# Optimization experiments

Hardware: AMD Instinct MI355X
Metric: run time of the kernel (lower is better)

Reference implementation:

```python
import jax, jax.numpy as jnp
import numpy as np

B, C, N, L = 64, 32, 500, 12
C_OUT = 32
C_CAT = 9 * C  # (order*(support_len+1)+1)*c_in = 288


def setup_inputs() -> dict:
    key = jax.random.key(0)
    ks = jax.random.split(key, 7)
    x = jax.random.normal(ks[0], (B, C, N, L), dtype=jnp.float32)
    # row-stochastic-ish adjacencies: scale by 1/N to keep hops numerically tame
    A0 = jax.random.uniform(ks[1], (N, N), dtype=jnp.float32) / N
    A1 = jax.random.uniform(ks[2], (N, N), dtype=jnp.float32) / N
    A2 = jax.random.uniform(ks[3], (N, N), dtype=jnp.float32) / N
    A3 = jax.random.uniform(ks[4], (B, N, N), dtype=jnp.float32) / N
    W = jax.random.normal(ks[5], (C_OUT, C_CAT), dtype=jnp.float32) * 0.05
    b = jax.random.normal(ks[6], (C_OUT,), dtype=jnp.float32) * 0.05
    return {"x": x, "A0": A0, "A1": A1, "A2": A2, "A3": A3, "W": W, "b": b}


def reference(x, A0, A1, A2, A3, W, b):
    # x: [B, C, N, L]; A0..A2: [N, N]; A3: [B, N, N]; W: [C_OUT, 9*C]; b: [C_OUT]
    def hop2(h, A):  # static adjacency
        return jnp.einsum('ncvl,vw->ncwl', h, A)

    def hop3(h, A):  # batched (dynamic) adjacency
        return jnp.einsum('ncvl,nvw->ncwl', h, A)

    out = [x]
    for A in (A0, A1, A2):
        x1 = hop2(x, A)
        x2 = hop2(x1, A)
        out.extend([x1, x2])
    x1 = hop3(x, A3)
    x2 = hop3(x1, A3)
    out.extend([x1, x2])

    h = jnp.concatenate(out, axis=1)  # [B, 9C, N, L]
    # 1x1 Conv2d == channel mixing matmul + bias
    h = jnp.einsum('ncvl,oc->novl', h, W) + b[None, :, None, None]
    # dropout in eval mode: identity
    return h
```

## Files before the change

kernel.cpp:

```cpp
#include <hip/hip_runtime.h>

typedef unsigned short u16;
typedef __bf16 bf16x8 __attribute__((ext_vector_type(8)));
typedef float f32x4 __attribute__((ext_vector_type(4)));
typedef const unsigned int __attribute__((address_space(1))) gu32;
typedef unsigned int __attribute__((address_space(3))) lu32;

#define NN 500
#define LLc 12
#define CC 32
#define MM 384
#define KP 512
#define MT 96
#define NT2 128
#define XS_S 40
#define AS_S 40
#define CT2_S 136
#define TS_S 384
#define AT_ELS 256000

__device__ __forceinline__ u16 f2bf(float f) {
    union { float f; unsigned u; } cv; cv.f = f;
    unsigned u = cv.u;
    u += 0x7fffu + ((u >> 16) & 1u);
    return (u16)(u >> 16);
}
__device__ __forceinline__ float bf2f(u16 s) {
    union { unsigned u; float f; } cv; cv.u = ((unsigned)s) << 16;
    return cv.f;
}

__global__ __launch_bounds__(256) void atrans_all(
    const float* __restrict__ A0, const float* __restrict__ A1,
    const float* __restrict__ A2, const float* __restrict__ A3,
    u16* __restrict__ At_s, u16* __restrict__ At_b)
{
    __shared__ u16 Ls[32 * 36];
    const int t = threadIdx.x;
    const int n0 = blockIdx.x * 32;
    const int k0 = blockIdx.y * 32;
    const int z = blockIdx.z;
    const float* Ab; u16* Ob;
    if (z == 0)      { Ab = A0; Ob = At_s; }
    else if (z == 1) { Ab = A1; Ob = At_s + (long)AT_ELS; }
    else if (z == 2) { Ab = A2; Ob = At_s + 2L * AT_ELS; }
    else             { Ab = A3 + (long)(z - 3) * NN * NN; Ob = At_b + (long)(z - 3) * AT_ELS; }
    {
        int vl = t >> 3, u = t & 7;
        float4 v = make_float4(0.f, 0.f, 0.f, 0.f);
        if (k0 + vl < NN && n0 + 4 * u + 4 <= NN)
            v = *(const float4*)(Ab + (long)(k0 + vl) * NN + n0 + 4 * u);
        int nb = 4 * u;
        Ls[(nb + 0) * 36 + vl] = f2bf(v.x);
        Ls[(nb + 1) * 36 + vl] = f2bf(v.y);
        Ls[(nb + 2) * 36 + vl] = f2bf(v.z);
        Ls[(nb + 3) * 36 + vl] = f2bf(v.w);
    }
    __syncthreads();
    {
        int row = t >> 3, u = t & 7;
        if (n0 + row < NN)
            *(uint2*)(Ob + (long)(n0 + row) * KP + k0 + 4 * u) = *(const uint2*)(&Ls[row * 36 + 4 * u]);
    }
}

__global__ __launch_bounds__(256) void xpose_kernel(
    const float* __restrict__ x, u16* __restrict__ Xt)
{
    __shared__ u16 Ls[MM * 36];
    const int t = threadIdx.x;
    const int v0 = blockIdx.x * 32;
    const int b  = blockIdx.y;
    #pragma unroll
    for (int j = 0; j < 12; ++j) {
        int f = t + 256 * j;
        int c = f / 96;
        int r = f - c * 96;
        int vl = r / 3;
        int l3 = (r - vl * 3) * 4;
        float4 v = make_float4(0.f, 0.f, 0.f, 0.f);
        if (v0 + vl < NN)
            v = *(const float4*)(x + ((long)b * CC + c) * (NN * LLc) + (long)(v0 + vl) * LLc + l3);
        int mb = (c * LLc + l3) * 36 + vl;
        Ls[mb]       = f2bf(v.x);
        Ls[mb + 36]  = f2bf(v.y);
        Ls[mb + 72]  = f2bf(v.z);
        Ls[mb + 108] = f2bf(v.w);
    }
    __syncthreads();
    #pragma unroll
    for (int j = 0; j < 12; ++j) {
        int f = t + 256 * j;
        int row = f >> 3, u = f & 7;
        *(uint2*)(Xt + ((long)b * MM + row) * KP + v0 + 4 * u) = *(const uint2*)(&Ls[row * 36 + 4 * u]);
    }
}

__global__ __launch_bounds__(256) void wpack_kernel(
    const float* __restrict__ W, u16* __restrict__ Wp)
{
    const int t = threadIdx.x;
    #pragma unroll 1
    for (int k = 0; k < 72; ++k) {
        int idx = t + 256 * k;
        int j    = idx & 7;
        int lane = (idx >> 3) & 63;
        int p    = (idx >> 9) & 1;
        int mt   = (idx >> 10) & 1;
        int g    = idx >> 11;
        int o  = mt * 16 + (lane & 15);
        int kk = g * 32 + (lane >> 4) * 8 + j;
        float wv = W[o * 288 + kk];
        u16 hi = f2bf(wv);
        Wp[idx] = (p == 0) ? hi : f2bf(wv - bf2f(hi));
    }
}

__global__ __launch_bounds__(256, 4) void hop_fast2(
    const u16* __restrict__ Xsrc, long x_gstride, long x_bstride, int x_rstride, int x_klim,
    const u16* __restrict__ At_s,
    const u16* __restrict__ At_b,
    u16* __restrict__ Hout, long h_gstride)
{
    __shared__ __align__(16) u16 smem[13056];
    u16* As = smem;
    u16* Xs = smem + 5120;
    u16* Ct = smem;

    const int t = threadIdx.x;
    const int lane = t & 63;
    const int wv = t >> 6;
    const int n0 = blockIdx.x * NT2;
    const int m0 = blockIdx.y * MT;
    const int g  = blockIdx.z & 3;
    const int b  = blockIdx.z >> 2;
    const int ln = lane & 15;
    const int q8 = (lane >> 4) * 8;

    const u16* Ab = (g < 3) ? (At_s + (long)g * AT_ELS) : (At_b + (long)b * AT_ELS);
    const u16* Xb = Xsrc + (long)g * x_gstride + (long)b * x_bstride;
    u16* Ob = Hout + (long)g * h_gstride + (long)b * ((long)MM * NN);

    uint2 pa[4], px[3];
    auto loadA = [&](int k0) {
        #pragma unroll
        for (int j = 0; j < 4; ++j) {
            int f = t + 256 * j;
            int n = f >> 3, u = f & 7;
            uint2 v = make_uint2(0u, 0u);
            if (n0 + n < NN)
                v = *(const uint2*)(Ab + (long)(n0 + n) * KP + k0 + 4 * u);
            pa[j] = v;
        }
    };
    auto loadX = [&](int k0) {
        #pragma unroll
        for (int j = 0; j < 3; ++j) {
            int f = t + 256 * j;
            int r = f >> 3, u = f & 7;
            int k = k0 + 4 * u;
            uint2 v = make_uint2(0u, 0u);
            if (k < x_klim)
                v = *(const uint2*)(Xb + (long)(m0 + r) * x_rstride + k);
            px[j] = v;
        }
    };

    f32x4 acc[2][6];
    #pragma unroll
    for (int ns = 0; ns < 2; ++ns)
        #pragma unroll
        for (int i = 0; i < 6; ++i)
            #pragma unroll
            for (int r = 0; r < 4; ++r) acc[ns][i][r] = 0.f;

    loadA(0);
    loadX(0);
    #pragma unroll 1
    for (int s = 0; s < 16; ++s) {
        __syncthreads();
        #pragma unroll
        for (int j = 0; j < 4; ++j) {
            int f = t + 256 * j;
            *(uint2*)(&As[(f >> 3) * AS_S + 4 * (f & 7)]) = pa[j];
        }
        #pragma unroll
        for (int j = 0; j < 3; ++j) {
            int f = t + 256 * j;
            *(uint2*)(&Xs[(f >> 3) * XS_S + 4 * (f & 7)]) = px[j];
        }
        if (s < 15) {
            loadA(32 * (s + 1));
            loadX(32 * (s + 1));
        }
        __syncthreads();
        bf16x8 af[6];
        #pragma unroll
        for (int i = 0; i < 6; ++i)
            af[i] = *(const bf16x8*)(&Xs[(i * 16 + ln) * XS_S + q8]);
        #pragma unroll
        for (int ns = 0; ns < 2; ++ns) {
            bf16x8 bfr = *(const bf16x8*)(&As[(wv * 32 + ns * 16 + ln) * AS_S + q8]);
            #pragma unroll
            for (int i = 0; i < 6; ++i)
                acc[ns][i] = __builtin_amdgcn_mfma_f32_16x16x32_bf16(af[i], bfr, acc[ns][i], 0, 0, 0);
        }
    }

    __syncthreads();
    #pragma unroll
    for (int ns = 0; ns < 2; ++ns) {
        int col = wv * 32 + ns * 16 + ln;
        #pragma unroll
        for (int i = 0; i < 6; ++i) {
            int rb = i * 16 + (lane >> 4) * 4;
            #pragma unroll
            for (int r = 0; r < 4; ++r)
                Ct[(rb + r) * CT2_S + col] = f2bf(acc[ns][i][r]);
        }
    }
    __syncthreads();
    #pragma unroll
    for (int j = 0; j < 12; ++j) {
        int f = t + 256 * j;
        int row = f >> 5, u = f & 31;
        int n = n0 + 4 * u;
        if (n < NN)
            *(uint2*)(Ob + (long)(m0 + row) * NN + n) = *(const uint2*)(&Ct[row * CT2_S + 4 * u]);
    }
}

__global__ __launch_bounds__(512, 4) void mix_mfma(
    const u16* __restrict__ Xt,
    const u16* __restrict__ H,
    const u16* __restrict__ Wp,
    const float* __restrict__ bias,
    float* __restrict__ out)
{
    __shared__ __align__(16) char smem[50176];
    u16*   Ls = (u16*)smem;
    float* Ct = (float*)smem;

    const int t   = threadIdx.x;
    const int wg  = blockIdx.y * 8 + blockIdx.x;
    const int swz = (wg & 7) * 64 + (wg >> 3);
    const int bx  = swz & 7;
    const int b   = swz >> 3;
    const int n0  = bx * 64;
    const int w    = t >> 6;
    const int lane = t & 63;
    const int kq   = lane >> 4;
    const int ln   = lane & 15;
    const int srow   = lane >> 3;
    const int schunk = (lane & 7) * 8;

    f32x4 acc[6][2];
    #pragma unroll
    for (int i = 0; i < 6; ++i)
        #pragma unroll
        for (int m = 0; m < 2; ++m)
            #pragma unroll
            for (int r = 0; r < 4; ++r) acc[i][m][r] = 0.f;

    #pragma unroll 1
    for (int g = 0; g < 9; ++g) {
        const u16* base; int rs;
        if (g == 0) { base = Xt + (long)b * (MM * KP); rs = KP; }
        else {
            int gg = g - 1;
            int buf = (gg & 1) ? 4 + (gg >> 1) : (gg >> 1);
            base = H + (long)buf * 12288000L + (long)b * 192000L; rs = NN;
        }
        __syncthreads();
        #pragma unroll
        for (int i = 0; i < 6; ++i) {
            int r0 = (w * 6 + i) * 8;
            const u16* src = base + (long)(r0 + srow) * rs + n0 + schunk;
            __builtin_amdgcn_global_load_lds((gu32*)src, (lu32*)(Ls + r0 * 64), 16, 0, 0);
        }
        asm volatile("s_waitcnt vmcnt(0)" ::: "memory");
        __syncthreads();
        uint4 wf[2][2];
        #pragma unroll
        for (int mt = 0; mt < 2; ++mt)
            #pragma unroll
            for (int p = 0; p < 2; ++p)
                wf[mt][p] = *(const uint4*)(Wp + ((((g * 2 + mt) * 2 + p) * 64 + lane) * 8));
        #pragma unroll
        for (int i = 0; i < 6; ++i) {
            int ct = w * 6 + i;
            int off0 = kq * 6144 + (ct >> 2) * 64 + (ct & 3) * 16 + ln;
            union { u16 s[8]; bf16x8 v; } fb;
            #pragma unroll
            for (int j = 0; j < 8; ++j) fb.s[j] = Ls[off0 + j * 768];
            #pragma unroll
            for (int mt = 0; mt < 2; ++mt) {
                acc[i][mt] = __builtin_amdgcn_mfma_f32_16x16x32_bf16(*(const bf16x8*)&wf[mt][0], fb.v, acc[i][mt], 0, 0, 0);
                acc[i][mt] = __builtin_amdgcn_mfma_f32_16x16x32_bf16(*(const bf16x8*)&wf[mt][1], fb.v, acc[i][mt], 0, 0, 0);
            }
        }
    }

    #pragma unroll
    for (int mt = 0; mt < 2; ++mt) {
        __syncthreads();
        #pragma unroll
        for (int i = 0; i < 6; ++i) {
            int col = (w * 6 + i) * 16 + ln;
            #pragma unroll
            for (int r = 0; r < 4; ++r)
                Ct[(kq * 4 + r) * 781 + col] = acc[i][mt][r];
        }
        __syncthreads();
        int o16 = t >> 5, u = t & 31;
        int og = mt * 16 + o16;
        float bs = bias[og];
        float* ob = out + (((long)b * CC + og) * NN + n0) * 12L;
        #pragma unroll
        for (int j2 = 0; j2 < 2; ++j2) {
            int n = u + 32 * j2;
            if (n0 + n < NN) {
                float v[12];
                #pragma unroll
                for (int l = 0; l < 12; ++l) v[l] = Ct[o16 * 781 + l * 64 + n] + bs;
                #pragma unroll
                for (int q = 0; q < 3; ++q)
                    *(float4*)(ob + (long)n * 12 + q * 4) = *(const float4*)&v[q * 4];
            }
        }
    }
}

__global__ __launch_bounds__(256, 3) void mix_all(
    const u16* __restrict__ Xt,
    const u16* __restrict__ H,
    const float* __restrict__ W,
    const float* __restrict__ bias,
    float* __restrict__ out)
{
    __shared__ __align__(16) float smem[96 * 36 + 288 * 33];
    float* ts = smem;
    float* Ws = smem + 96 * 36;

    const int t  = threadIdx.x;
    const int b  = blockIdx.y;
    const int w0 = blockIdx.x * 32;
    const int o  = t & 31;
    const int wq = t >> 5;
    const int w4 = wq * 4;
    const long HBUF = (long)64 * MM * NN;

    #pragma unroll
    for (int j = 0; j < 36; ++j) {
        int f = t + 256 * j;
        int oo = f & 31, ci = f >> 5;
        Ws[ci * 33 + oo] = W[oo * 288 + ci];
    }

    float acc[4][12];
    #pragma unroll
    for (int k = 0; k < 4; ++k)
        #pragma unroll
        for (int l = 0; l < 12; ++l) acc[k][l] = 0.f;

    uint2 px[3];
    auto loadq = [&](int q) {
        int g = q >> 2, c0 = (q & 3) << 3;
        const u16* base; int rs;
        if (g == 0) { base = Xt + (long)b * (MM * KP); rs = KP; }
        else {
            int gg = g - 1, i = gg >> 1;
            int buf = (gg & 1) ? 4 + i : i;
            base = H + (long)buf * HBUF + (long)b * ((long)MM * NN); rs = NN;
        }
        int m0c = c0 * 12;
        #pragma unroll
        for (int j = 0; j < 3; ++j) {
            int f = t + 256 * j;
            int r = f >> 3, u = f & 7;
            px[j] = *(const uint2*)(base + (long)(m0c + r) * rs + w0 + 4 * u);
        }
    };

    loadq(0);
    #pragma unroll 1
    for (int q = 0; q < 36; ++q) {
        __syncthreads();
        #pragma unroll
        for (int j = 0; j < 3; ++j) {
            int f = t + 256 * j;
            int r = f >> 3, u = f & 7;
            uint2 raw = px[j];
            float4 v = make_float4(bf2f((u16)(raw.x & 0xffffu)), bf2f((u16)(raw.x >> 16)),
                                   bf2f((u16)(raw.y & 0xffffu)), bf2f((u16)(raw.y >> 16)));
            *(float4*)(&ts[r * 36 + 4 * u]) = v;
        }
        if (q < 35) loadq(q + 1);
        __syncthreads();
        int g = q >> 2, c0 = (q & 3) << 3;
        #pragma unroll 1
        for (int cl = 0; cl < 8; ++cl) {
            float wgt = Ws[(g * 32 + c0 + cl) * 33 + o];
            #pragma unroll
            for (int l = 0; l < 12; ++l) {
                float4 h = *(const float4*)(&ts[(cl * 12 + l) * 36 + w4]);
                acc[0][l] += wgt * h.x;
                acc[1][l] += wgt * h.y;
                acc[2][l] += wgt * h.z;
                acc[3][l] += wgt * h.w;
            }
        }
    }

    #pragma unroll 1
    for (int r = 0; r < 4; ++r) {
        __syncthreads();
        if ((o >> 3) == r) {
            int ol = o & 7;
            #pragma unroll
            for (int k = 0; k < 4; ++k)
                #pragma unroll
                for (int l = 0; l < 12; ++l)
                    ts[ol * 388 + (w4 + k) * 12 + l] = acc[k][l];
        }
        __syncthreads();
        #pragma unroll
        for (int j = 0; j < 3; ++j) {
            int f4 = t + 256 * j;
            int ol = f4 / 96;
            int rem = f4 - ol * 96;
            int w  = rem / 3;
            int lq = rem - w * 3;
            if (w0 + w < NN) {
                float4 v = *(const float4*)(&ts[ol * 388 + w * 12 + lq * 4]);
                float bs = bias[r * 8 + ol];
                v.x += bs; v.y += bs; v.z += bs; v.w += bs;
                *(float4*)(out + (((long)b * CC + r * 8 + ol) * NN + w0 + w) * LLc + lq * 4) = v;
            }
        }
    }
}

__global__ __launch_bounds__(256, 4) void hop_fast(
    const u16* __restrict__ Xsrc, long x_bstride, int x_rstride, int x_klim,
    const u16* __restrict__ At,   long a_bstride,
    u16* __restrict__ hout)
{
    __shared__ __align__(16) u16 smem[13056];
    u16* As = smem;
    u16* Xs = smem + 5120;
    u16* Ct = smem;

    const int t = threadIdx.x;
    const int lane = t & 63;
    const int wv = t >> 6;
    const int n0 = blockIdx.x * NT2;
    const int m0 = blockIdx.y * MT;
    const int b  = blockIdx.z;
    const int ln = lane & 15;
    const int q8 = (lane >> 4) * 8;

    const u16* Ab = At + (long)b * a_bstride;
    const u16* Xb = Xsrc + (long)b * x_bstride;

    uint2 pa[4], px[3];
    auto loadA = [&](int k0) {
        #pragma unroll
        for (int j = 0; j < 4; ++j) {
            int f = t + 256 * j;
            int n = f >> 3, u = f & 7;
            uint2 v = make_uint2(0u, 0u);
            if (n0 + n < NN)
                v = *(const uint2*)(Ab + (long)(n0 + n) * KP + k0 + 4 * u);
            pa[j] = v;
        }
    };
    auto loadX = [&](int k0) {
        #pragma unroll
        for (int j = 0; j < 3; ++j) {
            int f = t + 256 * j;
            int r = f >> 3, u = f & 7;
            int k = k0 + 4 * u;
            uint2 v = make_uint2(0u, 0u);
            if (k < x_klim)
                v = *(const uint2*)(Xb + (long)(m0 + r) * x_rstride + k);
            px[j] = v;
        }
    };

    f32x4 acc[2][6];
    #pragma unroll
    for (int ns = 0; ns < 2; ++ns)
        #pragma unroll
        for (int i = 0; i < 6; ++i)
            #pragma unroll
            for (int r = 0; r < 4; ++r) acc[ns][i][r] = 0.f;

    loadA(0);
    loadX(0);
    #pragma unroll 1
    for (int s = 0; s < 16; ++s) {
        __syncthreads();
        #pragma unroll
        for (int j = 0; j < 4; ++j) {
            int f = t + 256 * j;
            *(uint2*)(&As[(f >> 3) * AS_S + 4 * (f & 7)]) = pa[j];
        }
        #pragma unroll
        for (int j = 0; j < 3; ++j) {
            int f = t + 256 * j;
            *(uint2*)(&Xs[(f >> 3) * XS_S + 4 * (f & 7)]) = px[j];
        }
        if (s < 15) {
            loadA(32 * (s + 1));
            loadX(32 * (s + 1));
        }
        __syncthreads();
        bf16x8 af[6];
        #pragma unroll
        for (int i = 0; i < 6; ++i)
            af[i] = *(const bf16x8*)(&Xs[(i * 16 + ln) * XS_S + q8]);
        #pragma unroll
        for (int ns = 0; ns < 2; ++ns) {
            bf16x8 bfr = *(const bf16x8*)(&As[(wv * 32 + ns * 16 + ln) * AS_S + q8]);
            #pragma unroll
            for (int i = 0; i < 6; ++i)
                acc[ns][i] = __builtin_amdgcn_mfma_f32_16x16x32_bf16(af[i], bfr, acc[ns][i], 0, 0, 0);
        }
    }

    __syncthreads();
    #pragma unroll
    for (int ns = 0; ns < 2; ++ns) {
        int col = wv * 32 + ns * 16 + ln;
        #pragma unroll
        for (int i = 0; i < 6; ++i) {
            int rb = i * 16 + (lane >> 4) * 4;
            #pragma unroll
            for (int r = 0; r < 4; ++r)
                Ct[(rb + r) * CT2_S + col] = f2bf(acc[ns][i][r]);
        }
    }
    __syncthreads();
    u16* Ob = hout + (long)b * ((long)MM * NN);
    #pragma unroll
    for (int j = 0; j < 12; ++j) {
        int f = t + 256 * j;
        int row = f >> 5, u = f & 31;
        int n = n0 + 4 * u;
        if (n < NN)
            *(uint2*)(Ob + (long)(m0 + row) * NN + n) = *(const uint2*)(&Ct[row * CT2_S + 4 * u]);
    }
}

__global__ __launch_bounds__(256, 2) void mix_kernel(
    const float* __restrict__ x,
    const u16* __restrict__ h1,
    const u16* __restrict__ h2,
    const float* __restrict__ W,
    const float* __restrict__ bias,
    int blk1, int blk2,
    float* __restrict__ out, int init)
{
    __shared__ __align__(16) float smem[CC * TS_S + 3 * 1056];
    float* ts = smem;
    float* Ws = smem + CC * TS_S;

    const int t = threadIdx.x;
    const int b = blockIdx.y;
    const int w0 = blockIdx.x * 32;
    const int o  = t & 15;
    const int wg = (t >> 4) & 7;
    const int lh = t >> 7;

    #pragma unroll
    for (int j = 0; j < 4; ++j) {
        int f = t + 256 * j;
        int oo = f & 31, c = f >> 5;
        Ws[c * 33 + oo]        = W[oo * 288 + blk1 * 32 + c];
        Ws[1056 + c * 33 + oo] = W[oo * 288 + blk2 * 32 + c];
        if (init) Ws[2112 + c * 33 + oo] = W[oo * 288 + c];
    }

    float acc2[2][4][6];
    #pragma unroll
    for (int a = 0; a < 2; ++a)
        #pragma unroll
        for (int q = 0; q < 4; ++q)
            #pragma unroll
            for (int l = 0; l < 6; ++l) acc2[a][q][l] = 0.f;

    auto stage_h = [&](const u16* h) {
        #pragma unroll
        for (int j = 0; j < 12; ++j) {
            int f = t + 256 * j;
            int row = f >> 3, u = f & 7;
            int w = w0 + 4 * u;
            uint2 raw = make_uint2(0u, 0u);
            if (w < NN)
                raw = *(const uint2*)(h + ((long)b * MM + row) * NN + w);
            int c = row / 12;
            int l = row - c * 12;
            float* dst = &ts[c * TS_S + l * 32 + 4 * u];
            dst[0] = bf2f((u16)(raw.x & 0xffffu));
            dst[1] = bf2f((u16)(raw.x >> 16));
            dst[2] = bf2f((u16)(raw.y & 0xffffu));
            dst[3] = bf2f((u16)(raw.y >> 16));
        }
    };
    auto accum = [&](const float* Wg) {
        for (int c = 0; c < CC; ++c) {
            float w1 = Wg[c * 33 + o];
            float w2 = Wg[c * 33 + o + 16];
            #pragma unroll
            for (int l6 = 0; l6 < 6; ++l6) {
                const float4 hv = *(const float4*)(&ts[c * TS_S + (lh * 6 + l6) * 32 + wg * 4]);
                acc2[0][0][l6] += w1 * hv.x;
                acc2[0][1][l6] += w1 * hv.y;
                acc2[0][2][l6] += w1 * hv.z;
                acc2[0][3][l6] += w1 * hv.w;
                acc2[1][0][l6] += w2 * hv.x;
                acc2[1][1][l6] += w2 * hv.y;
                acc2[1][2][l6] += w2 * hv.z;
                acc2[1][3][l6] += w2 * hv.w;
            }
        }
    };

    if (init) {
        #pragma unroll
        for (int j = 0; j < 12; ++j) {
            int f = t + 256 * j;
            int c = f / 96;
            int r = f - c * 96;
            int w = r / 3;
            int q = r - w * 3;
            float4 v = make_float4(0.f, 0.f, 0.f, 0.f);
            if (w0 + w < NN)
                v = *(const float4*)(x + ((long)b * CC + c) * (NN * LLc) + (long)(w0 + w) * LLc + q * 4);
            float* dst = &ts[c * TS_S + (q * 4) * 32 + w];
            dst[0]  = v.x; dst[32] = v.y; dst[64] = v.z; dst[96] = v.w;
        }
        __syncthreads();
        accum(Ws + 2112);
        __syncthreads();
    }
    stage_h(h1);
    __syncthreads();
    accum(Ws);
    __syncthreads();
    stage_h(h2);
    __syncthreads();
    accum(Ws + 1056);

    #pragma unroll
    for (int oh = 0; oh < 2; ++oh) {
        int oo = o + 16 * oh;
        float bs = init ? bias[oo] : 0.f;
        #pragma unroll
        for (int q = 0; q < 4; ++q) {
            int w = w0 + wg * 4 + q;
            if (w < NN) {
                float* op = out + ((long)b * CC + oo) * (NN * LLc) + (long)w * LLc + lh * 6;
                #pragma unroll
                for (int p = 0; p < 3; ++p) {
                    float2* pp = (float2*)op + p;
                    float2 v;
                    if (init) {
                        v.x = bs + acc2[oh][q][2 * p];
                        v.y = bs + acc2[oh][q][2 * p + 1];
                    } else {
                        v = *pp;
                        v.x += acc2[oh][q][2 * p];
                        v.y += acc2[oh][q][2 * p + 1];
                    }
                    *pp = v;
                }
            }
        }
    }
}

extern "C" void kernel_launch(void* const* d_in, const int* in_sizes, int n_in,
                              void* d_out, int out_size, void* d_ws, size_t ws_size,
                              hipStream_t stream) {
    const float* x    = (const float*)d_in[0];
    const float* A0   = (const float*)d_in[1];
    const float* A1   = (const float*)d_in[2];
    const float* A2   = (const float*)d_in[3];
    const float* A3   = (const float*)d_in[4];
    const float* W    = (const float*)d_in[5];
    const float* bias = (const float*)d_in[6];
    float* out = (float*)d_out;
    char* ws = (char*)d_ws;

    const size_t HBUF_ELS  = (size_t)64 * MM * NN;
    const size_t H8_BYTES  = 8 * HBUF_ELS * 2;
    const size_t AT_BYTES  = (size_t)AT_ELS * 2;
    const size_t A3T_BYTES = 64 * AT_BYTES;
    const size_t XT_BYTES  = (size_t)64 * MM * KP * 2;
    const size_t need2 = H8_BYTES + 3 * AT_BYTES + A3T_BYTES + XT_BYTES;
    const size_t WPK_BYTES = 36864;
    const size_t need3 = need2 + WPK_BYTES;

    dim3 blk(256);

    if (ws_size >= need3) {
        u16* Hb   = (u16*)ws;
        u16* At_s = (u16*)(ws + H8_BYTES);
        u16* A3t  = At_s + 3L * AT_ELS;
        u16* Xt   = (u16*)(ws + H8_BYTES + 3 * AT_BYTES + A3T_BYTES);
        u16* Wpk  = (u16*)(ws + need2);

        atrans_all<<<dim3(16, 16, 67), blk, 0, stream>>>(A0, A1, A2, A3, At_s, A3t);
        xpose_kernel<<<dim3(16, 64), blk, 0, stream>>>(x, Xt);
        wpack_kernel<<<dim3(1), blk, 0, stream>>>(W, Wpk);
        hop_fast2<<<dim3(4, 4, 256), blk, 0, stream>>>(
            Xt, 0L, (long)MM * KP, KP, KP, At_s, A3t, Hb, (long)HBUF_ELS);
        hop_fast2<<<dim3(4, 4, 256), blk, 0, stream>>>(
            Hb, (long)HBUF_ELS, (long)MM * NN, NN, NN, At_s, A3t,
            Hb + 4 * HBUF_ELS, (long)HBUF_ELS);
        mix_mfma<<<dim3(8, 64), dim3(512), 0, stream>>>(Xt, Hb, Wpk, bias, out);
        return;
    }

    if (ws_size >= need2) {
        u16* H    = (u16*)ws;
        u16* At_s = (u16*)(ws + H8_BYTES);
        u16* A3t  = At_s + 3L * AT_ELS;
        u16* Xt   = (u16*)(ws + H8_BYTES + 3 * AT_BYTES + A3T_BYTES);

        atrans_all<<<dim3(16, 16, 67), blk, 0, stream>>>(A0, A1, A2, A3, At_s, A3t);
        xpose_kernel<<<dim3(16, 64), blk, 0, stream>>>(x, Xt);
        hop_fast2<<<dim3(4, 4, 256), blk, 0, stream>>>(
            Xt, 0L, (long)MM * KP, KP, KP, At_s, A3t, H, (long)HBUF_ELS);
        hop_fast2<<<dim3(4, 4, 256), blk, 0, stream>>>(
            H, (long)HBUF_ELS, (long)MM * NN, NN, NN, At_s, A3t,
            H + 4 * HBUF_ELS, (long)HBUF_ELS);
        mix_all<<<dim3(16, 64), blk, 0, stream>>>(Xt, H, W, bias, out);
        return;
    }

    const size_t H_BYTES   = HBUF_ELS * 2;
    const size_t need_at   = 2 * H_BYTES + 3 * AT_BYTES + A3T_BYTES;
    const size_t need_full = need_at + XT_BYTES;

    u16* H1 = (u16*)ws;
    u16* H2 = (u16*)(ws + H_BYTES);
    u16* At0 = (u16*)(ws + 2 * H_BYTES);
    u16* A3t = At0 + 3L * AT_ELS;
    u16* Xt  = (u16*)(ws + need_at);
    (void)need_full;

    dim3 fgrid(4, 4, 64);
    dim3 mgrid(16, 64);

    xpose_kernel<<<dim3(16, 64), blk, 0, stream>>>(x, Xt);
    atrans_all<<<dim3(16, 16, 67), blk, 0, stream>>>(A0, A1, A2, A3, At0, A3t);

    const long XT_BS = (long)MM * KP;
    const long H_BS  = (long)MM * NN;
    u16* Atp[4] = {At0, At0 + (long)AT_ELS, At0 + 2L * AT_ELS, A3t};

    for (int i = 0; i < 4; ++i) {
        long a_bs = (i == 3) ? (long)AT_ELS : 0;
        hop_fast<<<fgrid, blk, 0, stream>>>(Xt, XT_BS, KP, KP, Atp[i], a_bs, H1);
        hop_fast<<<fgrid, blk, 0, stream>>>(H1, H_BS, NN, NN, Atp[i], a_bs, H2);
        mix_kernel<<<mgrid, blk, 0, stream>>>(i == 0 ? x : nullptr, H1, H2, W, bias,
                                              2 * i + 1, 2 * i + 2, out, i == 0 ? 1 : 0);
    }
}
```

Baseline: 437.9 us.

## Double hop kernel M-tile to 192 rows and swizzle block order

The hop GEMM kernel now computes 192 output rows per block instead of 96. Each block loads the adjacency tile once and reuses each A fragment across 12 MFMA row tiles, which halves A traffic and the block count. The linear block index is remapped so neighbouring blocks share the same batch/graph slice, likely to improve L2 locality across XCDs. In exchange the kernel needs twice the accumulator registers, the launch-bounds occupancy hint drops from 4 to 3, and the epilogue is split into two LDS staging passes.

```diff
diff --git a/kernel.cpp b/kernel.cpp
--- a/kernel.cpp
+++ b/kernel.cpp
@@ -116,7 +116,7 @@
     }
 }
 
-__global__ __launch_bounds__(256, 4) void hop_fast2(
+__global__ __launch_bounds__(256, 3) void hop_fast3(
     const u16* __restrict__ Xsrc, long x_gstride, long x_bstride, int x_rstride, int x_klim,
     const u16* __restrict__ At_s,
     const u16* __restrict__ At_b,
@@ -130,10 +130,15 @@
     const int t = threadIdx.x;
     const int lane = t & 63;
     const int wv = t >> 6;
-    const int n0 = blockIdx.x * NT2;
-    const int m0 = blockIdx.y * MT;
-    const int g  = blockIdx.z & 3;
-    const int b  = blockIdx.z >> 2;
+    const int f0 = blockIdx.x + 4 * blockIdx.y + 8 * blockIdx.z;
+    const int w  = (f0 & 7) * 256 + (f0 >> 3);
+    const int bx = w & 3;
+    const int by = (w >> 2) & 1;
+    const int zc = w >> 3;
+    const int g  = zc & 3;
+    const int b  = zc >> 2;
+    const int n0 = bx * NT2;
+    const int m0 = by * 192;
     const int ln = lane & 15;
     const int q8 = (lane >> 4) * 8;
 
@@ -141,7 +146,7 @@
     const u16* Xb = Xsrc + (long)g * x_gstride + (long)b * x_bstride;
     u16* Ob = Hout + (long)g * h_gstride + (long)b * ((long)MM * NN);
 
-    uint2 pa[4], px[3];
+    uint2 pa[4], px[6];
     auto loadA = [&](int k0) {
         #pragma unroll
         for (int j = 0; j < 4; ++j) {
@@ -155,7 +160,7 @@
     };
     auto loadX = [&](int k0) {
         #pragma unroll
-        for (int j = 0; j < 3; ++j) {
+        for (int j = 0; j < 6; ++j) {
             int f = t + 256 * j;
             int r = f >> 3, u = f & 7;
             int k = k0 + 4 * u;
@@ -166,11 +171,11 @@
         }
     };
 
-    f32x4 acc[2][6];
+    f32x4 acc[2][12];
     #pragma unroll
     for (int ns = 0; ns < 2; ++ns)
         #pragma unroll
-        for (int i = 0; i < 6; ++i)
+        for (int i = 0; i < 12; ++i)
             #pragma unroll
             for (int r = 0; r < 4; ++r) acc[ns][i][r] = 0.f;
 
@@ -185,7 +190,7 @@
             *(uint2*)(&As[(f >> 3) * AS_S + 4 * (f & 7)]) = pa[j];
         }
         #pragma unroll
-        for (int j = 0; j < 3; ++j) {
+        for (int j = 0; j < 6; ++j) {
             int f = t + 256 * j;
             *(uint2*)(&Xs[(f >> 3) * XS_S + 4 * (f & 7)]) = px[j];
         }
@@ -194,39 +199,39 @@
             loadX(32 * (s + 1));
         }
         __syncthreads();
-        bf16x8 af[6];
-        #pragma unroll
-        for (int i = 0; i < 6; ++i)
-            af[i] = *(const bf16x8*)(&Xs[(i * 16 + ln) * XS_S + q8]);
+        bf16x8 b0 = *(const bf16x8*)(&As[(wv * 32 + ln) * AS_S + q8]);
+        bf16x8 b1 = *(const bf16x8*)(&As[(wv * 32 + 16 + ln) * AS_S + q8]);
+        #pragma unroll
+        for (int i = 0; i < 12; ++i) {
+            bf16x8 af = *(const bf16x8*)(&Xs[(i * 16 + ln) * XS_S + q8]);
+            acc[0][i] = __builtin_amdgcn_mfma_f32_16x16x32_bf16(af, b0, acc[0][i], 0, 0, 0);
+            acc[1][i] = __builtin_amdgcn_mfma_f32_16x16x32_bf16(af, b1, acc[1][i], 0, 0, 0);
+        }
+    }
+
+    #pragma unroll
+    for (int h = 0; h < 2; ++h) {
+        __syncthreads();
         #pragma unroll
         for (int ns = 0; ns < 2; ++ns) {
-            bf16x8 bfr = *(const bf16x8*)(&As[(wv * 32 + ns * 16 + ln) * AS_S + q8]);
-            #pragma unroll
-            for (int i = 0; i < 6; ++i)
-                acc[ns][i] = __builtin_amdgcn_mfma_f32_16x16x32_bf16(af[i], bfr, acc[ns][i], 0, 0, 0);
-        }
-    }
-
-    __syncthreads();
-    #pragma unroll
-    for (int ns = 0; ns < 2; ++ns) {
-        int col = wv * 32 + ns * 16 + ln;
-        #pragma unroll
-        for (int i = 0; i < 6; ++i) {
-            int rb = i * 16 + (lane >> 4) * 4;
-            #pragma unroll
-            for (int r = 0; r < 4; ++r)
-                Ct[(rb + r) * CT2_S + col] = f2bf(acc[ns][i][r]);
-        }
-    }
-    __syncthreads();
-    #pragma unroll
-    for (int j = 0; j < 12; ++j) {
-        int f = t + 256 * j;
-        int row = f >> 5, u = f & 31;
-        int n = n0 + 4 * u;
-        if (n < NN)
-            *(uint2*)(Ob + (long)(m0 + row) * NN + n) = *(const uint2*)(&Ct[row * CT2_S + 4 * u]);
+            int col = wv * 32 + ns * 16 + ln;
+            #pragma unroll
+            for (int i6 = 0; i6 < 6; ++i6) {
+                int rb = i6 * 16 + (lane >> 4) * 4;
+                #pragma unroll
+                for (int r = 0; r < 4; ++r)
+                    Ct[(rb + r) * CT2_S + col] = f2bf(acc[ns][h * 6 + i6][r]);
+            }
+        }
+        __syncthreads();
+        #pragma unroll
+        for (int j = 0; j < 12; ++j) {
+            int f = t + 256 * j;
+            int row = f >> 5, u = f & 31;
+            int n = n0 + 4 * u;
+            if (n < NN)
+                *(uint2*)(Ob + (long)(m0 + h * 96 + row) * NN + n) = *(const uint2*)(&Ct[row * CT2_S + 4 * u]);
+        }
     }
 }
 
@@ -704,6 +709,7 @@
     const size_t need3 = need2 + WPK_BYTES;
 
     dim3 blk(256);
+    dim3 hgrid(4, 2, 256);
 
     if (ws_size >= need3) {
         u16* Hb   = (u16*)ws;
@@ -715,9 +721,9 @@
         atrans_all<<<dim3(16, 16, 67), blk, 0, stream>>>(A0, A1, A2, A3, At_s, A3t);
         xpose_kernel<<<dim3(16, 64), blk, 0, stream>>>(x, Xt);
         wpack_kernel<<<dim3(1), blk, 0, stream>>>(W, Wpk);
-        hop_fast2<<<dim3(4, 4, 256), blk, 0, stream>>>(
+        hop_fast3<<<hgrid, blk, 0, stream>>>(
             Xt, 0L, (long)MM * KP, KP, KP, At_s, A3t, Hb, (long)HBUF_ELS);
-        hop_fast2<<<dim3(4, 4, 256), blk, 0, stream>>>(
+        hop_fast3<<<hgrid, blk, 0, stream>>>(
             Hb, (long)HBUF_ELS, (long)MM * NN, NN, NN, At_s, A3t,
             Hb + 4 * HBUF_ELS, (long)HBUF_ELS);
         mix_mfma<<<dim3(8, 64), dim3(512), 0, stream>>>(Xt, Hb, Wpk, bias, out);
@@ -732,9 +738,9 @@
 
         atrans_all<<<dim3(16, 16, 67), blk, 0, stream>>>(A0, A1, A2, A3, At_s, A3t);
         xpose_kernel<<<dim3(16, 64), blk, 0, stream>>>(x, Xt);
-        hop_fast2<<<dim3(4, 4, 256), blk, 0, stream>>>(
+        hop_fast3<<<hgrid, blk, 0, stream>>>(
             Xt, 0L, (long)MM * KP, KP, KP, At_s, A3t, H, (long)HBUF_ELS);
-        hop_fast2<<<dim3(4, 4, 256), blk, 0, stream>>>(
+        hop_fast3<<<hgrid, blk, 0, stream>>>(
             H, (long)HBUF_ELS, (long)MM * NN, NN, NN, At_s, A3t,
             H + 4 * HBUF_ELS, (long)HBUF_ELS);
         mix_all<<<dim3(16, 64), blk, 0, stream>>>(Xt, H, W, bias, out);
```

Measured after the change: 394.1 us. 10.0% less time.
